# Kernel tuning notes

Hardware: AMD Instinct MI355X
Metric: run time of the kernel (lower is better)

The kernel has to match this reference:

```python
import jax, jax.numpy as jnp
import numpy as np

BN_EPS = 1e-5

def mish(x):
    return x * jnp.tanh(jax.nn.softplus(x))

def setup_inputs() -> dict:
    key = jax.random.key(0)
    k1, k2, k3 = jax.random.split(key, 3)
    B, C, D, N = 16, 512, 512, 2048
    x = jax.random.normal(k1, (B, C, N), dtype=jnp.float32)
    W = jax.random.normal(k2, (D, C), dtype=jnp.float32) * (1.0 / np.sqrt(C))
    gamma = jnp.ones((D,), dtype=jnp.float32)
    bn_beta = jnp.zeros((D,), dtype=jnp.float32)
    beta = jax.random.normal(k3, (1,), dtype=jnp.float32) * 0.1
    return {"x": x, "W": W, "gamma": gamma, "bn_beta": bn_beta, "beta": beta}

def reference(x, W, gamma, bn_beta, beta):
    # 1x1 conv: [B,C,N] -> [B,D,N]
    q = jnp.einsum('dc,bcn->bdn', W, x)
    # BatchNorm1d (training-mode batch stats, biased variance) over (B, N) per channel
    mean = jnp.mean(q, axis=(0, 2), keepdims=True)
    var = jnp.mean(jnp.square(q - mean), axis=(0, 2), keepdims=True)
    q = (q - mean) * jax.lax.rsqrt(var + BN_EPS)
    q = q * gamma[None, :, None] + bn_beta[None, :, None]
    h = mish(q)                                   # proj_key  [B,D,N]; proj_query = h^T [B,N,D]
    energy = jnp.einsum('bdn,bdm->bnm', h, h)     # bmm(Q, Q^T) -> [B,N,N]
    attn = jax.nn.softmax(energy, axis=-1)
    out_x = jnp.einsum('bdm,bnm->bdn', h, attn)   # bmm(proj_key, attn^T)
    return beta[0] * out_x + h
```

## Files before the change

kernel.cpp:

```cpp
#include <hip/hip_runtime.h>
#include <cstdint>
#include <cstddef>

#define B_DIM 16
#define C_DIM 512
#define D_DIM 512
#define N_DIM 2048

typedef _Float16 half8  __attribute__((ext_vector_type(8)));
typedef float    floatx4 __attribute__((ext_vector_type(4)));

__device__ __forceinline__ void gload_lds16(const _Float16* g, _Float16* l)
{
    __builtin_amdgcn_global_load_lds((const __attribute__((address_space(1))) void*)g,
                                     (__attribute__((address_space(3))) void*)l,
                                     16, 0, 0);
}

template<int EPI, typename OutT>
__global__ __launch_bounds__(512)
void gemm_nt256(const _Float16* __restrict__ A, size_t strideA,
                const _Float16* __restrict__ Bm, size_t strideB,
                OutT* __restrict__ Cm, size_t strideC,
                int M, int Ncols, int K,
                const float* __restrict__ beta_ptr,
                const _Float16* __restrict__ Hm, size_t strideH)
{
    constexpr int BK = 64;
    __shared__ _Float16 sA[2][256 * BK];
    __shared__ _Float16 sB[2][256 * BK];

    const int gx = gridDim.x, gy = gridDim.y;
    const int nwg = gx * gy * gridDim.z;
    int flat = blockIdx.x + gx * (blockIdx.y + gy * blockIdx.z);
    const int q8 = nwg >> 3;
    flat = (flat & 7) * q8 + (flat >> 3);
    const int bx = flat % gx;
    const int by = (flat / gx) % gy;
    const int bz = flat / (gx * gy);

    const _Float16* Ab = A  + (size_t)bz * strideA;
    const _Float16* Bb = Bm + (size_t)bz * strideB;
    const int m0 = bx * 256;
    const int n0 = by * 256;

    const int tid  = threadIdx.x;
    const int lane = tid & 63;
    const int wid  = tid >> 6;
    const int wr   = wid >> 2;
    const int wc   = wid & 3;
    const int fr   = lane & 15;
    const int hi   = lane >> 4;

    const int srow = (wid << 3) + (lane >> 3);
    const int sk   = ((lane & 7) ^ (srow & 7)) * 8;

    const _Float16* gA = Ab + (size_t)(m0 + srow) * K + sk;
    const _Float16* gB = Bb + (size_t)(n0 + srow) * K + sk;
    const int ldsbase = (wid << 3) * BK;

    auto stage = [&](int buf, int kt) {
        const size_t ko = (size_t)kt * BK;
        _Float16* la = &sA[buf][ldsbase];
        _Float16* lb = &sB[buf][ldsbase];
        const _Float16* ga = gA + ko;
        const _Float16* gb = gB + ko;
        #pragma unroll
        for (int p = 0; p < 4; ++p) {
            gload_lds16(ga + (size_t)(p * 64) * K, la + p * 64 * BK);
            gload_lds16(gb + (size_t)(p * 64) * K, lb + p * 64 * BK);
        }
    };

    floatx4 acc[8][4] = {};

    auto compute = [&](int buf) {
        const _Float16* fA = &sA[buf][(wr * 128 + fr) * BK];
        const _Float16* fB = &sB[buf][(wc * 64 + fr) * BK];
        #pragma unroll
        for (int ks = 0; ks < 2; ++ks) {
            const int ch = ((ks * 4 + hi) ^ (fr & 7)) * 8;
            half8 bf[4];
            #pragma unroll
            for (int n = 0; n < 4; ++n) bf[n] = *(const half8*)(fB + n * 16 * BK + ch);
            #pragma unroll
            for (int mh = 0; mh < 2; ++mh) {
                half8 af[4];
                #pragma unroll
                for (int m = 0; m < 4; ++m) af[m] = *(const half8*)(fA + (mh * 4 + m) * 16 * BK + ch);
                __builtin_amdgcn_s_setprio(1);
                #pragma unroll
                for (int m = 0; m < 4; ++m)
                    #pragma unroll
                    for (int n = 0; n < 4; ++n)
                        acc[mh * 4 + m][n] = __builtin_amdgcn_mfma_f32_16x16x32_f16(
                            af[m], bf[n], acc[mh * 4 + m][n], 0, 0, 0);
                __builtin_amdgcn_s_setprio(0);
            }
        }
    };

    const int nt = K / BK;
    stage(0, 0);
    for (int t = 0; t < nt; ++t) {
        asm volatile("s_waitcnt lgkmcnt(0)" ::: "memory");
        __builtin_amdgcn_s_barrier();
        __builtin_amdgcn_sched_barrier(0);
        if (t + 1 < nt) {
            stage((t + 1) & 1, t + 1);
            asm volatile("s_waitcnt vmcnt(8)" ::: "memory");
        } else {
            asm volatile("s_waitcnt vmcnt(0)" ::: "memory");
        }
        __builtin_amdgcn_sched_barrier(0);
        __builtin_amdgcn_s_barrier();
        __builtin_amdgcn_sched_barrier(0);
        compute(t & 1);
    }

    float beta = 0.0f;
    const _Float16* Hb = nullptr;
    if (EPI == 1) { beta = beta_ptr[0]; Hb = Hm + (size_t)bz * strideH; }
    OutT* Cb = Cm + (size_t)bz * strideC;

    #pragma unroll
    for (int i = 0; i < 8; ++i) {
        const int rowb = m0 + wr * 128 + i * 16 + (hi << 2);
        #pragma unroll
        for (int j = 0; j < 4; ++j) {
            const int col = n0 + wc * 64 + j * 16 + fr;
            #pragma unroll
            for (int r = 0; r < 4; ++r) {
                size_t idx = (size_t)(rowb + r) * Ncols + col;
                float v = acc[i][j][r];
                if (EPI == 1) v = beta * v + (float)Hb[idx];
                Cb[idx] = (OutT)v;
            }
        }
    }
}

__global__ void convert_w_kernel(const float* __restrict__ W, _Float16* __restrict__ Wh, int n)
{
    int i = blockIdx.x * 256 + threadIdx.x;
    if (i < n) Wh[i] = (_Float16)W[i];
}

__global__ void transpose_convert_x(const float* __restrict__ x, _Float16* __restrict__ xT)
{
    __shared__ float tile[32][33];
    const int bz = blockIdx.z;
    const int n0 = blockIdx.x * 32;
    const int c0 = blockIdx.y * 32;
    const int tx = threadIdx.x, ty = threadIdx.y;
    const float* xb = x + (size_t)bz * C_DIM * N_DIM;
    #pragma unroll
    for (int j = 0; j < 4; ++j)
        tile[ty + j * 8][tx] = xb[(size_t)(c0 + ty + j * 8) * N_DIM + n0 + tx];
    __syncthreads();
    _Float16* xtb = xT + (size_t)bz * N_DIM * C_DIM;
    #pragma unroll
    for (int j = 0; j < 4; ++j)
        xtb[(size_t)(n0 + ty + j * 8) * C_DIM + c0 + tx] = (_Float16)tile[tx][ty + j * 8];
}

__global__ __launch_bounds__(256)
void bn_stats(const _Float16* __restrict__ q, const float* __restrict__ gamma,
              const float* __restrict__ bn_beta, float2* __restrict__ stats)
{
    const int d = blockIdx.x;
    const int tid = threadIdx.x;
    float s = 0.f, ss = 0.f;
    for (int b = 0; b < B_DIM; ++b) {
        const _Float16* row = q + ((size_t)b * D_DIM + d) * N_DIM;
        half8 v = *(const half8*)(row + tid * 8);
        #pragma unroll
        for (int j = 0; j < 8; ++j) {
            float f = (float)v[j];
            s += f; ss += f * f;
        }
    }
    #pragma unroll
    for (int off = 32; off; off >>= 1) {
        s  += __shfl_down(s,  off, 64);
        ss += __shfl_down(ss, off, 64);
    }
    __shared__ float red[8];
    const int wv = tid >> 6;
    if ((tid & 63) == 0) { red[wv] = s; red[4 + wv] = ss; }
    __syncthreads();
    if (tid == 0) {
        s  = red[0] + red[1] + red[2] + red[3];
        ss = red[4] + red[5] + red[6] + red[7];
        const float inv = 1.0f / (float)(B_DIM * N_DIM);
        float mean = s * inv;
        float var  = ss * inv - mean * mean;
        float scale = gamma[d] * rsqrtf(var + 1e-5f);
        stats[d] = make_float2(scale, bn_beta[d] - mean * scale);
    }
}

__device__ __forceinline__ float mishf(float v)
{
    float t = __expf(fminf(v, 30.0f));
    float u = 1.0f + t;
    u *= u;
    return v * (u - 1.0f) * __builtin_amdgcn_rcpf(u + 1.0f);
}

__global__ void bn_mish(const _Float16* __restrict__ q, const float2* __restrict__ stats,
                        _Float16* __restrict__ h, _Float16* __restrict__ hT)
{
    __shared__ float tile[32][33];
    const int bz = blockIdx.z;
    const int n0 = blockIdx.x * 32;
    const int d0 = blockIdx.y * 32;
    const int tx = threadIdx.x, ty = threadIdx.y;
    const _Float16* qb = q + (size_t)bz * D_DIM * N_DIM;
    _Float16* hb = h + (size_t)bz * D_DIM * N_DIM;
    #pragma unroll
    for (int j = 0; j < 4; ++j) {
        int d = d0 + ty + j * 8;
        float2 sc = stats[d];
        float v  = (float)qb[(size_t)d * N_DIM + n0 + tx];
        float hv = mishf(v * sc.x + sc.y);
        tile[ty + j * 8][tx] = hv;
        hb[(size_t)d * N_DIM + n0 + tx] = (_Float16)hv;
    }
    __syncthreads();
    _Float16* htb = hT + (size_t)bz * N_DIM * D_DIM;
    #pragma unroll
    for (int j = 0; j < 4; ++j)
        htb[(size_t)(n0 + ty + j * 8) * D_DIM + d0 + tx] = (_Float16)tile[tx][ty + j * 8];
}

__global__ __launch_bounds__(256)
void softmax_rows(const _Float16* __restrict__ energy, size_t strideE,
                  _Float16* __restrict__ attn, size_t strideAt)
{
    const int wid  = threadIdx.x >> 6;
    const int lane = threadIdx.x & 63;
    const int n = blockIdx.x * 4 + wid;
    const int b = blockIdx.y;
    const _Float16* row = energy + (size_t)b * strideE + (size_t)n * N_DIM;
    _Float16*      orow = attn   + (size_t)b * strideAt + (size_t)n * N_DIM;
    float f[32];
    #pragma unroll
    for (int w = 0; w < 4; ++w) {
        half8 v = *(const half8*)(row + w * 512 + lane * 8);
        #pragma unroll
        for (int j = 0; j < 8; ++j) f[w * 8 + j] = (float)v[j];
    }
    float mx = f[0];
    #pragma unroll
    for (int k = 1; k < 32; ++k) mx = fmaxf(mx, f[k]);
    #pragma unroll
    for (int off = 1; off < 64; off <<= 1) mx = fmaxf(mx, __shfl_xor(mx, off, 64));
    float s = 0.f;
    #pragma unroll
    for (int k = 0; k < 32; ++k) { f[k] = __expf(f[k] - mx); s += f[k]; }
    #pragma unroll
    for (int off = 1; off < 64; off <<= 1) s += __shfl_xor(s, off, 64);
    const float inv = 1.0f / s;
    #pragma unroll
    for (int w = 0; w < 4; ++w) {
        half8 o;
        #pragma unroll
        for (int j = 0; j < 8; ++j) o[j] = (_Float16)(f[w * 8 + j] * inv);
        *(half8*)(orow + w * 512 + lane * 8) = o;
    }
}

extern "C" void kernel_launch(void* const* d_in, const int* in_sizes, int n_in,
                              void* d_out, int out_size, void* d_ws, size_t ws_size,
                              hipStream_t stream)
{
    const float* x       = (const float*)d_in[0];
    const float* W       = (const float*)d_in[1];
    const float* gamma   = (const float*)d_in[2];
    const float* bn_beta = (const float*)d_in[3];
    const float* beta    = (const float*)d_in[4];
    float* out = (float*)d_out;

    char* ws = (char*)d_ws;
    size_t off = 0;
    auto take = [&](size_t bytes) -> char* {
        char* p = ws + off;
        off = (off + bytes + 255) & ~(size_t)255;
        return p;
    };

    _Float16* xT    = (_Float16*)take((size_t)B_DIM * N_DIM * C_DIM * 2);
    _Float16* q     = (_Float16*)take((size_t)B_DIM * D_DIM * N_DIM * 2);
    _Float16* h     = (_Float16*)take((size_t)B_DIM * D_DIM * N_DIM * 2);
    _Float16* Wh    = (_Float16*)take((size_t)D_DIM * C_DIM * 2);
    float2*   stats = (float2*)  take((size_t)D_DIM * sizeof(float2));
    _Float16* hT    = xT;

    const size_t eSz = (size_t)N_DIM * N_DIM * 2;
    const size_t fixedEnd = off;
    const int full = (ws_size >= fixedEnd + (size_t)B_DIM * eSz + 1024) ? 1 : 0;
    _Float16* energy = (_Float16*)take(full ? (size_t)B_DIM * eSz : eSz);
    _Float16* attn   = energy;

    convert_w_kernel<<<dim3((D_DIM * C_DIM + 255) / 256), dim3(256), 0, stream>>>(W, Wh, D_DIM * C_DIM);
    transpose_convert_x<<<dim3(N_DIM / 32, C_DIM / 32, B_DIM), dim3(32, 8), 0, stream>>>(x, xT);
    gemm_nt256<0, _Float16><<<dim3(D_DIM / 256, N_DIM / 256, B_DIM), dim3(512), 0, stream>>>(
        Wh, 0, xT, (size_t)N_DIM * C_DIM, q, (size_t)D_DIM * N_DIM,
        D_DIM, N_DIM, C_DIM, nullptr, nullptr, 0);
    bn_stats<<<dim3(D_DIM), dim3(256), 0, stream>>>(q, gamma, bn_beta, stats);
    bn_mish<<<dim3(N_DIM / 32, D_DIM / 32, B_DIM), dim3(32, 8), 0, stream>>>(q, stats, h, hT);

    if (full) {
        gemm_nt256<0, _Float16><<<dim3(N_DIM / 256, N_DIM / 256, B_DIM), dim3(512), 0, stream>>>(
            hT, (size_t)N_DIM * D_DIM, hT, (size_t)N_DIM * D_DIM, energy, (size_t)N_DIM * N_DIM,
            N_DIM, N_DIM, D_DIM, nullptr, nullptr, 0);
        softmax_rows<<<dim3(N_DIM / 4, B_DIM), dim3(256), 0, stream>>>(
            energy, (size_t)N_DIM * N_DIM, attn, (size_t)N_DIM * N_DIM);
        gemm_nt256<1, float><<<dim3(D_DIM / 256, N_DIM / 256, B_DIM), dim3(512), 0, stream>>>(
            h, (size_t)D_DIM * N_DIM, attn, (size_t)N_DIM * N_DIM, out, (size_t)D_DIM * N_DIM,
            D_DIM, N_DIM, N_DIM, beta, h, (size_t)D_DIM * N_DIM);
    } else {
        for (int b = 0; b < B_DIM; ++b) {
            const _Float16* hTb = hT + (size_t)b * N_DIM * D_DIM;
            const _Float16* hb  = h  + (size_t)b * D_DIM * N_DIM;
            gemm_nt256<0, _Float16><<<dim3(N_DIM / 256, N_DIM / 256, 1), dim3(512), 0, stream>>>(
                hTb, 0, hTb, 0, energy, 0, N_DIM, N_DIM, D_DIM, nullptr, nullptr, 0);
            softmax_rows<<<dim3(N_DIM / 4, 1), dim3(256), 0, stream>>>(energy, 0, attn, 0);
            gemm_nt256<1, float><<<dim3(D_DIM / 256, N_DIM / 256, 1), dim3(512), 0, stream>>>(
                hb, 0, attn, 0, out + (size_t)b * D_DIM * N_DIM, 0,
                D_DIM, N_DIM, N_DIM, beta, hb, 0);
        }
    }
}
```

Before: 276.6 us.

## Interleave split global-to-LDS loads across eight compute phases per two k-tiles

Replaces the stage-then-compute double-buffer loop with an 8-phase schedule per pair of k-tiles. Each phase loads its A/B fragments, issues a slice of the next tile's global_load_lds, runs 16 MFMAs and synchronizes. Prefetches are spread finely so memory traffic overlaps MFMA work instead of bunching before each compute. The cost is many more barriers per tile and fragile vmcnt bookkeeping; it also assumes an even tile count.

```diff
diff --git a/kernel.cpp b/kernel.cpp
--- a/kernel.cpp
+++ b/kernel.cpp
@@ -16,6 +16,34 @@
                                      (__attribute__((address_space(3))) void*)l,
                                      16, 0, 0);
 }
+
+#define PHASE(BUF, MH, KS, STAGES, VM)                                               \
+    {                                                                                 \
+        const _Float16* fA_ = &sA[BUF][(wr * 128 + (MH) * 64 + fr) * BK];             \
+        const _Float16* fB_ = &sB[BUF][(wc * 64 + fr) * BK];                          \
+        const int ch_ = (((KS) * 4 + hi) ^ (fr & 7)) * 8;                             \
+        half8 af_[4], bf_[4];                                                         \
+        _Pragma("unroll")                                                             \
+        for (int m_ = 0; m_ < 4; ++m_) af_[m_] = *(const half8*)(fA_ + m_ * 16 * BK + ch_); \
+        _Pragma("unroll")                                                             \
+        for (int n_ = 0; n_ < 4; ++n_) bf_[n_] = *(const half8*)(fB_ + n_ * 16 * BK + ch_); \
+        STAGES;                                                                       \
+        __builtin_amdgcn_s_barrier();                                                 \
+        asm volatile("s_waitcnt lgkmcnt(0)" ::: "memory");                            \
+        __builtin_amdgcn_sched_barrier(0);                                            \
+        __builtin_amdgcn_s_setprio(1);                                                \
+        _Pragma("unroll")                                                             \
+        for (int m_ = 0; m_ < 4; ++m_)                                                \
+            _Pragma("unroll")                                                         \
+            for (int n_ = 0; n_ < 4; ++n_)                                            \
+                acc[(MH) * 4 + m_][n_] = __builtin_amdgcn_mfma_f32_16x16x32_f16(      \
+                    af_[m_], bf_[n_], acc[(MH) * 4 + m_][n_], 0, 0, 0);               \
+        __builtin_amdgcn_s_setprio(0);                                                \
+        if ((VM) == 0)      asm volatile("s_waitcnt vmcnt(0)" ::: "memory");          \
+        else if ((VM) == 2) asm volatile("s_waitcnt vmcnt(2)" ::: "memory");          \
+        __builtin_amdgcn_s_barrier();                                                 \
+        __builtin_amdgcn_sched_barrier(0);                                            \
+    }
 
 template<int EPI, typename OutT>
 __global__ __launch_bounds__(512)
@@ -59,63 +87,43 @@
     const _Float16* gB = Bb + (size_t)(n0 + srow) * K + sk;
     const int ldsbase = (wid << 3) * BK;
 
-    auto stage = [&](int buf, int kt) {
+    auto stageA = [&](int buf, int kt, int half) {
         const size_t ko = (size_t)kt * BK;
-        _Float16* la = &sA[buf][ldsbase];
-        _Float16* lb = &sB[buf][ldsbase];
-        const _Float16* ga = gA + ko;
-        const _Float16* gb = gB + ko;
-        #pragma unroll
-        for (int p = 0; p < 4; ++p) {
-            gload_lds16(ga + (size_t)(p * 64) * K, la + p * 64 * BK);
-            gload_lds16(gb + (size_t)(p * 64) * K, lb + p * 64 * BK);
-        }
+        #pragma unroll
+        for (int p = half; p < 4; p += 2)
+            gload_lds16(gA + ko + (size_t)(p * 64) * K, &sA[buf][ldsbase + p * 64 * BK]);
     };
+    auto stageB = [&](int buf, int kt, int half) {
+        const size_t ko = (size_t)kt * BK;
+        #pragma unroll
+        for (int p = half; p < 4; p += 2)
+            gload_lds16(gB + ko + (size_t)(p * 64) * K, &sB[buf][ldsbase + p * 64 * BK]);
+    };
 
     floatx4 acc[8][4] = {};
 
-    auto compute = [&](int buf) {
-        const _Float16* fA = &sA[buf][(wr * 128 + fr) * BK];
-        const _Float16* fB = &sB[buf][(wc * 64 + fr) * BK];
-        #pragma unroll
-        for (int ks = 0; ks < 2; ++ks) {
-            const int ch = ((ks * 4 + hi) ^ (fr & 7)) * 8;
-            half8 bf[4];
-            #pragma unroll
-            for (int n = 0; n < 4; ++n) bf[n] = *(const half8*)(fB + n * 16 * BK + ch);
-            #pragma unroll
-            for (int mh = 0; mh < 2; ++mh) {
-                half8 af[4];
-                #pragma unroll
-                for (int m = 0; m < 4; ++m) af[m] = *(const half8*)(fA + (mh * 4 + m) * 16 * BK + ch);
-                __builtin_amdgcn_s_setprio(1);
-                #pragma unroll
-                for (int m = 0; m < 4; ++m)
-                    #pragma unroll
-                    for (int n = 0; n < 4; ++n)
-                        acc[mh * 4 + m][n] = __builtin_amdgcn_mfma_f32_16x16x32_f16(
-                            af[m], bf[n], acc[mh * 4 + m][n], 0, 0, 0);
-                __builtin_amdgcn_s_setprio(0);
-            }
-        }
-    };
-
     const int nt = K / BK;
-    stage(0, 0);
-    for (int t = 0; t < nt; ++t) {
-        asm volatile("s_waitcnt lgkmcnt(0)" ::: "memory");
-        __builtin_amdgcn_s_barrier();
-        __builtin_amdgcn_sched_barrier(0);
-        if (t + 1 < nt) {
-            stage((t + 1) & 1, t + 1);
-            asm volatile("s_waitcnt vmcnt(8)" ::: "memory");
-        } else {
-            asm volatile("s_waitcnt vmcnt(0)" ::: "memory");
-        }
-        __builtin_amdgcn_sched_barrier(0);
-        __builtin_amdgcn_s_barrier();
-        __builtin_amdgcn_sched_barrier(0);
-        compute(t & 1);
+    const int niter = nt >> 1;
+
+    stageA(0, 0, 0); stageA(0, 0, 1);
+    stageB(0, 0, 0); stageB(0, 0, 1);
+    stageA(1, 1, 0);
+    asm volatile("s_waitcnt vmcnt(2)" ::: "memory");
+    __builtin_amdgcn_s_barrier();
+    __builtin_amdgcn_sched_barrier(0);
+
+    for (int it = 0; it < niter; ++it) {
+        const int b = 2 * it + 1, c = 2 * it + 2, d = 2 * it + 3;
+        const bool lastc = (c >= nt);
+        const int vm_end = lastc ? 0 : 2;
+        PHASE(0, 0, 0, { stageA(1, b, 1); stageB(1, b, 0); }, -1)
+        PHASE(0, 0, 1, { stageB(1, b, 1); }, -1)
+        PHASE(0, 1, 0, { if (!lastc) stageA(0, c, 0); }, -1)
+        PHASE(0, 1, 1, {}, vm_end)
+        PHASE(1, 0, 0, { if (!lastc) { stageA(0, c, 1); stageB(0, c, 0); } }, -1)
+        PHASE(1, 0, 1, { if (!lastc) stageB(0, c, 1); }, -1)
+        PHASE(1, 1, 0, { if (!lastc) stageA(1, d, 0); }, -1)
+        PHASE(1, 1, 1, {}, vm_end)
     }
 
     float beta = 0.0f;
```

Result: slower. 289.1 us (+4.5%).
